# Kernel tuning notes

Measured on AMD Instinct MI355X. Metric: run time of the kernel, lower is better.

The kernel has to match this reference:

```python
import jax, jax.numpy as jnp
import numpy as np
import math

N, E, K_ORD = 30000, 60000, 6
D, H, DQK, PE_DIM, HYPER, MAX_K = 256, 8, 256, 128, 256, 10
DH = DQK // H    # per-head qk dim (dim_qk_head)
DVH = D // H     # per-head v dim  (dim_v_head)
M = E * K_ORD + N  # incidence messages + node self-loops


def _sin_pe(max_len, d):
    pos = np.arange(max_len)[:, None].astype(np.float32)
    div = np.exp(np.arange(0, d, 2).astype(np.float32) * (-math.log(10000.0) / d))
    pe = np.zeros((max_len, d), np.float32)
    pe[:, 0::2] = np.sin(pos * div)
    pe[:, 1::2] = np.cos(pos * div)
    return jnp.asarray(pe)


def _ln(x, g, b, eps=1e-5):
    mu = x.mean(-1, keepdims=True)
    var = ((x - mu) ** 2).mean(-1, keepdims=True)
    return (x - mu) * jax.lax.rsqrt(var + eps) * g + b


def _mlp(x, w1, b1, w2, b2):
    return jax.nn.relu(x @ w1 + b1) @ w2 + b2


def _forward(x_v, x_e, q_w1, q_b1, q_w2, q_b2, k_w, k_b, v_w, v_b,
             m1_w1, m1_b1, m1_w2, m1_b2, m2_w1, m2_b1, m2_w2, m2_b2,
             m3_w1, m3_b1, m3_w2, m3_b2, n1_g, n1_b, n2_g, n2_b, n3_g, n3_b,
             bias_v, edge_orders, edge_index):
    n = x_v.shape[0]
    # order-conditional positional MLP residual (pe1 at order 1 for nodes, edge_orders for edges)
    pe1 = _sin_pe(MAX_K + 1, D)
    x_v = x_v + _mlp(jnp.concatenate([_ln(x_v, n1_g, n1_b), jnp.broadcast_to(pe1[1], x_v.shape)], -1), m1_w1, m1_b1, m1_w2, m1_b2)
    x_e = x_e + _mlp(jnp.concatenate([_ln(x_e, n1_g, n1_b), pe1[edge_orders]], -1), m1_w1, m1_b1, m1_w2, m1_b2)

    # queries from PositionalMLP over positions {0, 1}
    q = _mlp(_sin_pe(2, PE_DIM), q_w1, q_b1, q_w2, q_b2)  # [2, DQK]
    q0 = q[0].reshape(H, DH)
    q1 = q[1].reshape(H, DH)

    tok = jnp.concatenate([x_e, x_v], 0)                    # [E+N, D], edges first
    k_all = tok @ k_w + k_b                                  # [E+N, 2*DQK]
    k0 = k_all[:, :DQK].reshape(-1, H, DH)
    k1 = k_all[:, DQK:].reshape(-1, H, DH)
    v = (tok @ v_w + v_b).reshape(-1, H, DVH)

    # global PMA: softmax over all edge+node tokens
    logit0 = jnp.einsum('hd,ehd->eh', q0, k0) / math.sqrt(DH)
    alpha0 = jax.nn.softmax(logit0, axis=0)
    att0 = jnp.einsum('eh,ehd->hd', alpha0, v).reshape(1, D)

    # segment PMA: leaky_relu -> scatter-softmax over messages per target node
    src, tgt = edge_index[0], edge_index[1]
    a = jnp.sum(k1 * q1[None], -1)                           # [E+N, H] (no sqrt scaling, per PMA)
    a = jax.nn.leaky_relu(a[src], 0.2)                       # [M, H]
    a_max = jax.ops.segment_max(a, tgt, num_segments=n)
    a = jnp.exp(a - a_max[tgt])
    a = a / jax.ops.segment_sum(a, tgt, num_segments=n)[tgt]
    att1 = jax.ops.segment_sum(v[src] * a[..., None], tgt, num_segments=n).reshape(n, D)

    pe2 = _sin_pe(2, D)
    att0 = att0 + _mlp(jnp.concatenate([_ln(att0, n2_g, n2_b), pe2[0:1]], -1), m2_w1, m2_b1, m2_w2, m2_b2)
    att1 = att1 + _mlp(jnp.concatenate([_ln(att1, n2_g, n2_b), jnp.broadcast_to(pe2[1], att1.shape)], -1), m2_w1, m2_b1, m2_w2, m2_b2)
    x = att0 + att1
    x = x + _mlp(_ln(x, n3_g, n3_b), m3_w1, m3_b1, m3_w2, m3_b2)
    return x + bias_v


def setup_inputs():
    key = jax.random.key(0)
    ks = jax.random.split(key, 64)
    idx = iter(range(64))
    def nrm(shape, fan_in=None):
        s = 1.0 if fan_in is None else 1.0 / math.sqrt(fan_in)
        return jax.random.normal(ks[next(idx)], shape, jnp.float32) * s
    inp = {}
    inp['x_v'] = nrm((N, D))
    inp['x_e'] = nrm((E, D))
    inp['edge_orders'] = jax.random.randint(ks[next(idx)], (E,), 2, MAX_K + 1)
    tgt_inc = jax.random.randint(ks[next(idx)], (E * K_ORD,), 0, N)
    src = jnp.concatenate([jnp.repeat(jnp.arange(E), K_ORD), E + jnp.arange(N)])
    tgt = jnp.concatenate([tgt_inc, jnp.arange(N)])
    inp['edge_index'] = jnp.stack([src, tgt]).astype(jnp.int32)
    inp['q_w1'] = nrm((PE_DIM, HYPER), PE_DIM); inp['q_b1'] = jnp.zeros((HYPER,), jnp.float32)
    inp['q_w2'] = nrm((HYPER, DQK), HYPER);     inp['q_b2'] = jnp.zeros((DQK,), jnp.float32)
    inp['k_w'] = nrm((D, 2 * DQK), D);          inp['k_b'] = jnp.zeros((2 * DQK,), jnp.float32)
    inp['v_w'] = nrm((D, D), D);                inp['v_b'] = jnp.zeros((D,), jnp.float32)
    inp['m1_w1'] = nrm((2 * D, HYPER), 2 * D);  inp['m1_b1'] = jnp.zeros((HYPER,), jnp.float32)
    inp['m1_w2'] = nrm((HYPER, D), HYPER);      inp['m1_b2'] = jnp.zeros((D,), jnp.float32)
    inp['m2_w1'] = nrm((2 * D, HYPER), 2 * D);  inp['m2_b1'] = jnp.zeros((HYPER,), jnp.float32)
    inp['m2_w2'] = nrm((HYPER, D), HYPER);      inp['m2_b2'] = jnp.zeros((D,), jnp.float32)
    inp['m3_w1'] = nrm((D, HYPER), D);          inp['m3_b1'] = jnp.zeros((HYPER,), jnp.float32)
    inp['m3_w2'] = nrm((HYPER, D), HYPER);      inp['m3_b2'] = jnp.zeros((D,), jnp.float32)
    for nm in ('n1', 'n2', 'n3'):
        inp[nm + '_g'] = jnp.ones((D,), jnp.float32)
        inp[nm + '_b'] = jnp.zeros((D,), jnp.float32)
    inp['bias_v'] = jnp.zeros((D,), jnp.float32)
    return inp


def reference(x_v, x_e, edge_orders, edge_index, q_w1, q_b1, q_w2, q_b2, k_w, k_b, v_w, v_b,
              m1_w1, m1_b1, m1_w2, m1_b2, m2_w1, m2_b1, m2_w2, m2_b2,
              m3_w1, m3_b1, m3_w2, m3_b2, n1_g, n1_b, n2_g, n2_b, n3_g, n3_b, bias_v):
    return _forward(x_v, x_e, q_w1, q_b1, q_w2, q_b2, k_w, k_b, v_w, v_b,
                    m1_w1, m1_b1, m1_w2, m1_b2, m2_w1, m2_b1, m2_w2, m2_b2,
                    m3_w1, m3_b1, m3_w2, m3_b2, n1_g, n1_b, n2_g, n2_b, n3_g, n3_b,
                    bias_v, edge_orders, edge_index)
```

## Files before the change

### kernel.cpp

```cpp
#include <hip/hip_runtime.h>
#include <hip/hip_bf16.h>

#define N_NODES 30000
#define N_EDGE  60000
#define T_TOK   90000
#define M_MSG   390000
#define DD      256
#define HH      8
#define AS      260
#define FUSED_BLKS 1407
#define HIST_BLKS  762
#define SCAT_BLKS 1524
#define RED_BLKS  176
#define ATT1_BLKS 7500

typedef unsigned short u16;
typedef unsigned int   u32;
typedef short s16x8 __attribute__((ext_vector_type(8)));
typedef float f32x4 __attribute__((ext_vector_type(4)));

constexpr size_t WS_V     = 0;
constexpr size_t WS_ALR   = WS_V    + (size_t)T_TOK * DD * 2;
constexpr size_t WS_CNT   = WS_ALR  + (size_t)T_TOK * HH * 4;
constexpr size_t WS_OFF   = WS_CNT  + (size_t)N_NODES * 4;
constexpr size_t WS_CUR   = WS_OFF  + (size_t)(N_NODES + 1) * 4;
constexpr size_t WS_MSRC  = WS_CUR  + (size_t)N_NODES * 4;
constexpr size_t WS_SMALL = ((WS_MSRC + (size_t)M_MSG * 4) + 255) & ~(size_t)255;

struct Small {
  u16 wts[16][256];
  float b0[8], b1f[8];
  float q[2][256];
  float pe_c1[11][256];
  float pc2[2][256];
  float gmaxv[8], ginv[8];
  float att0_vec[256];
  float att0_upd[256];
};
constexpr size_t WS_WTS  = (WS_SMALL + sizeof(Small) + 255) & ~(size_t)255;
constexpr size_t WS_PART = WS_WTS  + 7 * 65536 * 2;
constexpr size_t WS_PDEN = WS_PART + (size_t)FUSED_BLKS * 256 * 4;
constexpr size_t WS_PMAX = WS_PDEN + (size_t)FUSED_BLKS * 8 * 4;

__device__ __forceinline__ float bf2f(u16 a){ return __uint_as_float(((u32)a) << 16); }
__device__ __forceinline__ u32 pkbf(float lo, float hi){
  u32 r;
  asm("v_cvt_pk_bf16_f32 %0, %1, %2" : "=v"(r) : "v"(lo), "v"(hi));
  return r;
}
__device__ __forceinline__ u16 f2bf(float f){ return (u16)pkbf(f, f); }
__device__ __forceinline__ float wredsum(float x){
  #pragma unroll
  for (int s = 32; s > 0; s >>= 1) x += __shfl_xor(x, s, 64);
  return x;
}
__device__ __forceinline__ float wredmax(float x){
  #pragma unroll
  for (int s = 32; s > 0; s >>= 1) x = fmaxf(x, __shfl_xor(x, s, 64));
  return x;
}

union U8 { s16x8 v; uint2 u2[2]; uint4 u4; };

template<bool SC>
__device__ __forceinline__ void mfma_tile64(const u16* sa, const u16* __restrict__ WT,
                                            const u16* __restrict__ wts, int tid,
                                            f32x4 fr[4][2], f32x4* fs)
{
  const int lane = tid & 63, w = tid >> 6;
  const int l15 = lane & 15, g = lane >> 4;
  const int slab = w >> 1, nt0 = (w & 1) * 2;
  #pragma unroll
  for (int m = 0; m < 4; m++)
    #pragma unroll
    for (int n = 0; n < 2; n++) fr[m][n] = (f32x4){0.f, 0.f, 0.f, 0.f};
  const u16* ap = sa + l15 * AS + 4 * g;
  const u16* bp = WT + (size_t)slab * 16384 + lane * 8;
  const bool do_s = SC && (w == 0);
  #pragma unroll 4
  for (int c = 0; c < 8; c++){
    const int k0 = c * 32;
    U8 a[4];
    #pragma unroll
    for (int m = 0; m < 4; m++){
      a[m].u2[0] = *(const uint2*)(ap + m * 16 * AS + k0);
      a[m].u2[1] = *(const uint2*)(ap + m * 16 * AS + k0 + 16);
    }
    U8 b[2];
    #pragma unroll
    for (int n = 0; n < 2; n++)
      b[n].u4 = *(const uint4*)(bp + (c * 4 + nt0 + n) * 512);
    #pragma unroll
    for (int n = 0; n < 2; n++)
      #pragma unroll
      for (int m = 0; m < 4; m++)
        fr[m][n] = __builtin_amdgcn_mfma_f32_16x16x32_bf16(a[m].v, b[n].v, fr[m][n], 0, 0, 0);
    if (do_s){
      U8 bs;
      bs.u4 = *(const uint4*)(wts + c * 512 + lane * 8);
      #pragma unroll
      for (int m = 0; m < 4; m++)
        fs[m] = __builtin_amdgcn_mfma_f32_16x16x32_bf16(a[m].v, bs.v, fs[m], 0, 0, 0);
    }
  }
}

__global__ void k_preq(const float* __restrict__ qw1, const float* __restrict__ qb1,
                       const float* __restrict__ qw2, const float* __restrict__ qb2,
                       const float* __restrict__ kb, Small* sm, int* cnt)
{
  __shared__ float s_qin[2][128];
  __shared__ float s_h1[2][256];
  __shared__ float s_q[2][256];
  int tid = threadIdx.x;
  int p = tid >> 8, col = tid & 255;
  for (int i = tid; i < N_NODES; i += 512) cnt[i] = 0;
  if (tid < 256) sm->att0_vec[tid] = 0.f;
  if (tid < 128){
    int i = tid >> 1;
    float dv = expf((float)(2 * i) * (-9.210340371976184f / 128.f));
    if (tid & 1){ s_qin[0][tid] = 1.f; s_qin[1][tid] = cosf(dv); }
    else        { s_qin[0][tid] = 0.f; s_qin[1][tid] = sinf(dv); }
  }
  __syncthreads();
  {
    float acc = qb1[col];
    for (int d = 0; d < 128; d++) acc = fmaf(s_qin[p][d], qw1[d * 256 + col], acc);
    s_h1[p][col] = fmaxf(acc, 0.f);
  }
  __syncthreads();
  {
    float acc = qb2[col];
    for (int k = 0; k < 256; k++) acc = fmaf(s_h1[p][k], qw2[k * 256 + col], acc);
    s_q[p][col] = acc;
    sm->q[p][col] = acc;
  }
  __syncthreads();
  if (tid < 8){
    float b0 = 0.f, b1 = 0.f;
    for (int i = 0; i < 32; i++){
      b0 = fmaf(kb[tid * 32 + i],       s_q[0][tid * 32 + i], b0);
      b1 = fmaf(kb[256 + tid * 32 + i], s_q[1][tid * 32 + i], b1);
    }
    sm->b0[tid] = b0; sm->b1f[tid] = b1;
  }
}

__global__ void k_prep(const float* __restrict__ kw, const float* __restrict__ m1w1,
                       const float* __restrict__ m2w1, Small* sm,
                       const float* __restrict__ s0, const float* __restrict__ s1,
                       const float* __restrict__ s2, const float* __restrict__ s3,
                       const float* __restrict__ s4, const float* __restrict__ s5,
                       const float* __restrict__ s6, u16* __restrict__ dst)
{
  int role = blockIdx.x, tid = threadIdx.x;
  if (role < 8){
    int d = role * 32 + (tid >> 3), h = tid & 7;
    float a0 = 0.f, a1 = 0.f;
    #pragma unroll
    for (int i = 0; i < 32; i++){
      a0 = fmaf(kw[d * 512 + h * 32 + i],       sm->q[0][h * 32 + i], a0);
      a1 = fmaf(kw[d * 512 + 256 + h * 32 + i], sm->q[1][h * 32 + i], a1);
    }
    int c = d >> 5, kk = d & 31;
    int g = (kk & 15) >> 2;
    int j = (kk & 3) + ((kk & 16) ? 4 : 0);
    u16* wf = &sm->wts[0][0];
    wf[(c * 64 + g * 16 + h) * 8 + j]     = f2bf(a0);
    wf[(c * 64 + g * 16 + 8 + h) * 8 + j] = f2bf(a1);
  } else if (role < 19){
    __shared__ float s_pe[256];
    int o = role - 8;
    {
      int i = tid >> 1;
      float dv = expf((float)(2 * i) * (-9.210340371976184f / 256.f));
      float ph = (float)o * dv;
      s_pe[tid] = (tid & 1) ? cosf(ph) : sinf(ph);
    }
    __syncthreads();
    float acc = 0.f;
    for (int d = 0; d < 256; d++) acc = fmaf(s_pe[d], m1w1[(256 + d) * 256 + tid], acc);
    sm->pe_c1[o][tid] = acc;
  } else if (role == 19){
    __shared__ float p0[256], p1[256];
    {
      int i = tid >> 1;
      float dv = expf((float)(2 * i) * (-9.210340371976184f / 256.f));
      p0[tid] = (tid & 1) ? 1.f : 0.f;
      p1[tid] = (tid & 1) ? cosf(dv) : sinf(dv);
    }
    __syncthreads();
    float a0 = 0.f, a1 = 0.f;
    for (int d = 0; d < 256; d++){
      float w = m2w1[(256 + d) * 256 + tid];
      a0 = fmaf(p0[d], w, a0);
      a1 = fmaf(p1[d], w, a1);
    }
    sm->pc2[0][tid] = a0; sm->pc2[1][tid] = a1;
  } else {
    int b = role - 20;
    int mat = b >> 5, rem = b & 31;
    int slab = rem >> 3, c = rem & 7;
    const float* S;
    switch (mat){ case 0: S = s0; break; case 1: S = s1; break; case 2: S = s2; break;
                  case 3: S = s3; break; case 4: S = s4; break; case 5: S = s5; break;
                  default: S = s6; }
    int nt = tid >> 6, lane = tid & 63;
    int l15 = lane & 15, g = lane >> 4;
    int n = slab * 64 + nt * 16 + l15;
    u16 tmp[8];
    #pragma unroll
    for (int j = 0; j < 8; j++){
      int k = c * 32 + g * 4 + (j & 3) + ((j >= 4) ? 16 : 0);
      tmp[j] = f2bf(S[(size_t)k * 256 + n]);
    }
    uint4 o;
    o.x = (u32)tmp[0] | ((u32)tmp[1] << 16);
    o.y = (u32)tmp[2] | ((u32)tmp[3] << 16);
    o.z = (u32)tmp[4] | ((u32)tmp[5] << 16);
    o.w = (u32)tmp[6] | ((u32)tmp[7] << 16);
    *(uint4*)(dst + (size_t)mat * 65536 + (size_t)((((slab * 8 + c) * 4 + nt) * 64 + lane) * 8)) = o;
  }
}

__global__ __launch_bounds__(512, 4) void k_fused1(
    const float* __restrict__ x_v, const float* __restrict__ x_e,
    const int* __restrict__ edge_orders,
    const u16* __restrict__ WTa, const u16* __restrict__ WTb, const u16* __restrict__ WTv,
    const float* __restrict__ b1, const float* __restrict__ b2,
    const float* __restrict__ n1g, const float* __restrict__ n1b,
    const float* __restrict__ vb,
    const Small* __restrict__ sm,
    u16* __restrict__ v, float* __restrict__ alr,
    float* __restrict__ part, float* __restrict__ pden, float* __restrict__ pmax,
    const int* __restrict__ tgt, int* __restrict__ cnt)
{
  if (blockIdx.x >= FUSED_BLKS){
    int m = (blockIdx.x - FUSED_BLKS) * 512 + threadIdx.x;
    if (m < M_MSG) atomicAdd(&cnt[tgt[m]], 1);
    return;
  }
  __shared__ u16 s_a[64 * AS];
  __shared__ int s_ord[64];
  __shared__ float s_l[64][8];
  __shared__ float s_e[8][64];
  __shared__ float s_p2[512];
  const int tid = threadIdx.x;
  const int t0  = blockIdx.x * 64;
  const int w = tid >> 6, lane = tid & 63;
  const int l15 = lane & 15, g = lane >> 4;
  const int cb = w * 32;

  uint2 xp[8];
  {
    float4 gg = *(const float4*)(n1g + lane * 4);
    float4 bb = *(const float4*)(n1b + lane * 4);
    #pragma unroll
    for (int i = 0; i < 8; i++){
      int r = w * 8 + i;
      int t = t0 + r;
      float4 xv = make_float4(0.f, 0.f, 0.f, 0.f);
      if (t < T_TOK){
        const float* p = (t < N_EDGE) ? (x_e + (size_t)t * DD) : (x_v + (size_t)(t - N_EDGE) * DD);
        xv = *(const float4*)(p + lane * 4);
      }
      xp[i].x = pkbf(xv.x, xv.y);
      xp[i].y = pkbf(xv.z, xv.w);
      float s  = xv.x + xv.y + xv.z + xv.w;
      float ss = fmaf(xv.x, xv.x, fmaf(xv.y, xv.y, fmaf(xv.z, xv.z, xv.w * xv.w)));
      s = wredsum(s); ss = wredsum(ss);
      float mu  = s * (1.f / 256.f);
      float var = fmaf(-mu, mu, ss * (1.f / 256.f));
      float rs  = rsqrtf(var + 1e-5f);
      uint2 p2;
      p2.x = pkbf(fmaf((xv.x - mu) * rs, gg.x, bb.x), fmaf((xv.y - mu) * rs, gg.y, bb.y));
      p2.y = pkbf(fmaf((xv.z - mu) * rs, gg.z, bb.z), fmaf((xv.w - mu) * rs, gg.w, bb.w));
      *(uint2*)(s_a + r * AS + lane * 4) = p2;
    }
  }
  if (tid < 64){
    int t = t0 + tid;
    s_ord[tid] = (t < N_EDGE) ? edge_orders[t] : 1;
  }
  __syncthreads();

  f32x4 fr[4][2];
  mfma_tile64<false>(s_a, WTa, nullptr, tid, fr, nullptr);
  __syncthreads();
  {
    float b1c[2];
    #pragma unroll
    for (int n = 0; n < 2; n++) b1c[n] = b1[cb + n * 16 + l15];
    #pragma unroll
    for (int m = 0; m < 4; m++){
      #pragma unroll
      for (int r = 0; r < 4; r++){
        int row = m * 16 + 4 * g + r;
        const float* per = &sm->pe_c1[s_ord[row]][0];
        #pragma unroll
        for (int n = 0; n < 2; n++){
          int col = cb + n * 16 + l15;
          s_a[row * AS + col] = f2bf(fmaxf(fr[m][n][r] + b1c[n] + per[col], 0.f));
        }
      }
    }
  }
  __syncthreads();
  mfma_tile64<false>(s_a, WTb, nullptr, tid, fr, nullptr);
  __syncthreads();
  {
    float b2c[2];
    #pragma unroll
    for (int n = 0; n < 2; n++) b2c[n] = b2[cb + n * 16 + l15];
    #pragma unroll
    for (int m = 0; m < 4; m++)
      #pragma unroll
      for (int n = 0; n < 2; n++){
        int col = cb + n * 16 + l15;
        #pragma unroll
        for (int r = 0; r < 4; r++){
          int row = m * 16 + 4 * g + r;
          s_a[row * AS + col] = f2bf(fr[m][n][r] + b2c[n]);
        }
      }
  }
  __syncthreads();
  #pragma unroll
  for (int i = 0; i < 8; i++){
    int r = w * 8 + i;
    uint2 q = *(const uint2*)(s_a + r * AS + lane * 4);
    uint2 xq = xp[i];
    uint2 o;
    o.x = pkbf(bf2f((u16)(q.x & 0xffff)) + bf2f((u16)(xq.x & 0xffff)),
               bf2f((u16)(q.x >> 16))    + bf2f((u16)(xq.x >> 16)));
    o.y = pkbf(bf2f((u16)(q.y & 0xffff)) + bf2f((u16)(xq.y & 0xffff)),
               bf2f((u16)(q.y >> 16))    + bf2f((u16)(xq.y >> 16)));
    *(uint2*)(s_a + r * AS + lane * 4) = o;
  }
  __syncthreads();
  f32x4 fs[4];
  #pragma unroll
  for (int m = 0; m < 4; m++) fs[m] = (f32x4){0.f, 0.f, 0.f, 0.f};
  mfma_tile64<true>(s_a, WTv, &sm->wts[0][0], tid, fr, fs);
  __syncthreads();
  {
    float vbc[2];
    #pragma unroll
    for (int n = 0; n < 2; n++) vbc[n] = vb[cb + n * 16 + l15];
    #pragma unroll
    for (int m = 0; m < 4; m++)
      #pragma unroll
      for (int n = 0; n < 2; n++){
        int col = cb + n * 16 + l15;
        #pragma unroll
        for (int r = 0; r < 4; r++){
          int row = m * 16 + 4 * g + r;
          s_a[row * AS + col] = f2bf(fr[m][n][r] + vbc[n]);
        }
      }
  }
  if (w == 0){
    #pragma unroll
    for (int m = 0; m < 4; m++)
      #pragma unroll
      for (int r = 0; r < 4; r++){
        int row = m * 16 + 4 * g + r;
        int t = t0 + row;
        int sc = l15;
        if (sc < 8){
          float lv = (t < T_TOK) ? (fs[m][r] + sm->b0[sc]) * 0.17677669529663687f : -1e30f;
          s_l[row][sc] = lv;
        } else if (t < T_TOK){
          float a_ = fs[m][r] + sm->b1f[sc - 8];
          alr[(size_t)t * 8 + sc - 8] = (a_ > 0.f) ? a_ : 0.2f * a_;
        }
      }
  }
  __syncthreads();
  {
    float lv = s_l[lane][w];
    float mxb = wredmax(lv);
    float e = __expf(lv - mxb);
    float den = wredsum(e);
    s_e[w][lane] = e;
    if (lane == 0){
      pden[(size_t)blockIdx.x * 8 + w] = den;
      pmax[(size_t)blockIdx.x * 8 + w] = mxb;
    }
  }
  __syncthreads();
  {
    int col = tid & 255, half = tid >> 8;
    int h = col >> 5;
    float acc = 0.f;
    #pragma unroll 8
    for (int r2 = half * 32; r2 < half * 32 + 32; r2++)
      acc = fmaf(s_e[h][r2], bf2f(s_a[r2 * AS + col]), acc);
    s_p2[tid] = acc;
  }
  __syncthreads();
  if (tid < 256) part[(size_t)blockIdx.x * 256 + tid] = s_p2[tid] + s_p2[tid + 256];
  #pragma unroll
  for (int i = 0; i < 4; i++){
    int ch = i * 512 + tid;
    int r = ch >> 5, c8 = (ch & 31) * 8;
    int t = t0 + r;
    if (t < T_TOK){
      uint2 q0 = *(const uint2*)(s_a + r * AS + c8);
      uint2 q1 = *(const uint2*)(s_a + r * AS + c8 + 4);
      *(uint4*)(v + (size_t)t * DD + c8) = make_uint4(q0.x, q0.y, q1.x, q1.y);
    }
  }
}

__global__ __launch_bounds__(1024) void k_scanbc(
    const int* __restrict__ cnt, int* __restrict__ off, int* __restrict__ cur,
    const float* __restrict__ pden, const float* __restrict__ pmax,
    Small* sm)
{
  int tid = threadIdx.x;
  if (blockIdx.x == 0){
    __shared__ int s_s[1024];
    int base = tid * 30;
    int s = 0;
    if (tid < 1000){
      for (int i = 0; i < 30; i++) s += cnt[base + i];
    }
    s_s[tid] = s;
    __syncthreads();
    for (int ofs = 1; ofs < 1024; ofs <<= 1){
      int v_ = (tid >= ofs) ? s_s[tid - ofs] : 0;
      __syncthreads();
      s_s[tid] += v_;
      __syncthreads();
    }
    if (tid < 1000){
      int run = (tid == 0) ? 0 : s_s[tid - 1];
      for (int i = 0; i < 30; i++){
        int c = cnt[base + i];
        off[base + i] = run; cur[base + i] = run;
        run += c;
      }
    }
    if (tid == 0) off[N_NODES] = M_MSG;
    return;
  }
  __shared__ float s_red[1024];
  __shared__ float s_g[8];
  {
    int h = tid & 7, bi = tid >> 3;
    float m = -1e30f;
    for (int b = bi; b < FUSED_BLKS; b += 128) m = fmaxf(m, pmax[(size_t)b * 8 + h]);
    s_red[tid] = m;
  }
  __syncthreads();
  for (int s = 512; s >= 8; s >>= 1){ if (tid < s) s_red[tid] = fmaxf(s_red[tid], s_red[tid + s]); __syncthreads(); }
  if (tid < 8) s_g[tid] = s_red[tid];
  __syncthreads();
  {
    int h = tid & 7, bi = tid >> 3;
    float gm = s_g[h];
    float s = 0.f;
    for (int b = bi; b < FUSED_BLKS; b += 128)
      s += pden[(size_t)b * 8 + h] * __expf(pmax[(size_t)b * 8 + h] - gm);
    s_red[tid] = s;
  }
  __syncthreads();
  for (int s = 512; s >= 8; s >>= 1){ if (tid < s) s_red[tid] += s_red[tid + s]; __syncthreads(); }
  if (tid < 8){ sm->gmaxv[tid] = s_g[tid]; sm->ginv[tid] = 1.f / s_red[tid]; }
}

__global__ __launch_bounds__(256) void k_scatred(
    const int* __restrict__ src, const int* __restrict__ tgt,
    int* __restrict__ cur, int* __restrict__ msrc,
    const float* __restrict__ part, const float* __restrict__ pmax,
    Small* sm)
{
  int b = blockIdx.x, tid = threadIdx.x;
  if (b < SCAT_BLKS){
    int m = b * 256 + tid;
    if (m < M_MSG){
      int slot = atomicAdd(&cur[tgt[m]], 1);
      msrc[slot] = src[m];
    }
    return;
  }
  int r = b - SCAT_BLKS;
  int h = tid >> 5;
  float gm = sm->gmaxv[h];
  float acc = 0.f;
  #pragma unroll
  for (int j = 0; j < 8; j++){
    int pb = r * 8 + j;
    if (pb < FUSED_BLKS)
      acc = fmaf(part[(size_t)pb * 256 + tid], __expf(pmax[(size_t)pb * 8 + h] - gm), acc);
  }
  atomicAdd(&sm->att0_vec[tid], acc);
}

__global__ __launch_bounds__(256) void k_att1(
    const int* __restrict__ off, const int* __restrict__ msrc,
    const float* __restrict__ alr, const u16* __restrict__ v,
    const float* __restrict__ m2w1, const float* __restrict__ m2b1,
    const float* __restrict__ m2w2, const float* __restrict__ m2b2,
    const float* __restrict__ n2g, const float* __restrict__ n2b,
    Small* sm, float* att1)
{
  int tid = threadIdx.x;
  if (blockIdx.x == ATT1_BLKS){
    __shared__ float s_ln[256], s_h[256], s_r8[8];
    float x = sm->att0_vec[tid] * sm->ginv[tid >> 5];
    float s1 = wredsum(x), s2 = wredsum(x * x);
    int wv = tid >> 6;
    if ((tid & 63) == 0){ s_r8[wv] = s1; s_r8[4 + wv] = s2; }
    __syncthreads();
    float tot  = s_r8[0] + s_r8[1] + s_r8[2] + s_r8[3];
    float tot2 = s_r8[4] + s_r8[5] + s_r8[6] + s_r8[7];
    float mu  = tot * (1.f / 256.f);
    float var = tot2 * (1.f / 256.f) - mu * mu;
    float rs  = rsqrtf(var + 1e-5f);
    s_ln[tid] = (x - mu) * rs * n2g[tid] + n2b[tid];
    __syncthreads();
    float acc = m2b1[tid] + sm->pc2[0][tid];
    for (int k = 0; k < 256; k++) acc = fmaf(s_ln[k], m2w1[k * 256 + tid], acc);
    s_h[tid] = fmaxf(acc, 0.f);
    __syncthreads();
    float o = m2b2[tid];
    for (int k = 0; k < 256; k++) o = fmaf(s_h[k], m2w2[k * 256 + tid], o);
    sm->att0_upd[tid] = x + o;
    return;
  }
  int n = blockIdx.x * 4 + (tid >> 6);
  if (n >= N_NODES) return;
  int l = tid & 63;
  int h = l >> 3;
  int beg = off[n], end = off[n + 1];
  float mxa = -1e30f, mxb = -1e30f;
  int i = beg;
  for (; i + 1 < end; i += 2){
    mxa = fmaxf(mxa, alr[(size_t)msrc[i] * 8 + h]);
    mxb = fmaxf(mxb, alr[(size_t)msrc[i + 1] * 8 + h]);
  }
  if (i < end) mxa = fmaxf(mxa, alr[(size_t)msrc[i] * 8 + h]);
  float mx = fmaxf(mxa, mxb);
  float den0 = 0.f, den1 = 0.f;
  float a0 = 0.f, a1 = 0.f, a2 = 0.f, a3 = 0.f;
  float c0 = 0.f, c1 = 0.f, c2 = 0.f, c3 = 0.f;
  i = beg;
  for (; i + 1 < end; i += 2){
    int s0 = msrc[i], s1 = msrc[i + 1];
    float w0 = __expf(alr[(size_t)s0 * 8 + h] - mx);
    float w1 = __expf(alr[(size_t)s1 * 8 + h] - mx);
    ushort4 r0 = *(const ushort4*)(v + (size_t)s0 * DD + l * 4);
    ushort4 r1 = *(const ushort4*)(v + (size_t)s1 * DD + l * 4);
    den0 += w0; den1 += w1;
    a0 = fmaf(w0, bf2f(r0.x), a0); c0 = fmaf(w1, bf2f(r1.x), c0);
    a1 = fmaf(w0, bf2f(r0.y), a1); c1 = fmaf(w1, bf2f(r1.y), c1);
    a2 = fmaf(w0, bf2f(r0.z), a2); c2 = fmaf(w1, bf2f(r1.z), c2);
    a3 = fmaf(w0, bf2f(r0.w), a3); c3 = fmaf(w1, bf2f(r1.w), c3);
  }
  if (i < end){
    int s0 = msrc[i];
    float w0 = __expf(alr[(size_t)s0 * 8 + h] - mx);
    ushort4 r0 = *(const ushort4*)(v + (size_t)s0 * DD + l * 4);
    den0 += w0;
    a0 = fmaf(w0, bf2f(r0.x), a0);
    a1 = fmaf(w0, bf2f(r0.y), a1);
    a2 = fmaf(w0, bf2f(r0.z), a2);
    a3 = fmaf(w0, bf2f(r0.w), a3);
  }
  float id_ = 1.f / (den0 + den1);
  *(float4*)(att1 + (size_t)n * DD + l * 4) =
      make_float4((a0 + c0) * id_, (a1 + c1) * id_, (a2 + c2) * id_, (a3 + c3) * id_);
}

__global__ __launch_bounds__(512, 4) void k_final(
    const float* att1,
    const u16* __restrict__ WT2a, const u16* __restrict__ WT2b,
    const u16* __restrict__ WT3a, const u16* __restrict__ WT3b,
    const float* __restrict__ m2b1, const float* __restrict__ m2b2,
    const float* __restrict__ m3b1, const float* __restrict__ m3b2,
    const float* __restrict__ n2g, const float* __restrict__ n2b,
    const float* __restrict__ n3g, const float* __restrict__ n3b,
    const float* __restrict__ bias_v, const Small* __restrict__ sm,
    float* out)
{
  __shared__ u16 s_a[64 * AS];
  const int tid = threadIdx.x;
  const int t0  = blockIdx.x * 64;
  const int w = tid >> 6, lane = tid & 63;
  const int l15 = lane & 15, g = lane >> 4;
  const int cb = w * 32;

  f32x4 xr[8];
  {
    float4 gg = *(const float4*)(n2g + lane * 4);
    float4 bb = *(const float4*)(n2b + lane * 4);
    #pragma unroll
    for (int i = 0; i < 8; i++){
      int r = w * 8 + i;
      int t = t0 + r;
      float4 xv = make_float4(0.f, 0.f, 0.f, 0.f);
      if (t < N_NODES) xv = *(const float4*)(att1 + (size_t)t * DD + lane * 4);
      xr[i][0] = xv.x; xr[i][1] = xv.y; xr[i][2] = xv.z; xr[i][3] = xv.w;
      float s  = xv.x + xv.y + xv.z + xv.w;
      float ss = fmaf(xv.x, xv.x, fmaf(xv.y, xv.y, fmaf(xv.z, xv.z, xv.w * xv.w)));
      s = wredsum(s); ss = wredsum(ss);
      float mu  = s * (1.f / 256.f);
      float var = fmaf(-mu, mu, ss * (1.f / 256.f));
      float rs  = rsqrtf(var + 1e-5f);
      uint2 p2;
      p2.x = pkbf(fmaf((xv.x - mu) * rs, gg.x, bb.x), fmaf((xv.y - mu) * rs, gg.y, bb.y));
      p2.y = pkbf(fmaf((xv.z - mu) * rs, gg.z, bb.z), fmaf((xv.w - mu) * rs, gg.w, bb.w));
      *(uint2*)(s_a + r * AS + lane * 4) = p2;
    }
  }
  __syncthreads();

  f32x4 fr[4][2];
  mfma_tile64<false>(s_a, WT2a, nullptr, tid, fr, nullptr);
  __syncthreads();
  {
    float bc[2], pc[2];
    #pragma unroll
    for (int n = 0; n < 2; n++){
      int col = cb + n * 16 + l15;
      bc[n] = m2b1[col]; pc[n] = sm->pc2[1][col];
    }
    #pragma unroll
    for (int m = 0; m < 4; m++)
      #pragma unroll
      for (int n = 0; n < 2; n++){
        int col = cb + n * 16 + l15;
        #pragma unroll
        for (int r = 0; r < 4; r++){
          int row = m * 16 + 4 * g + r;
          s_a[row * AS + col] = f2bf(fmaxf(fr[m][n][r] + bc[n] + pc[n], 0.f));
        }
      }
  }
  __syncthreads();
  mfma_tile64<false>(s_a, WT2b, nullptr, tid, fr, nullptr);
  __syncthreads();
  {
    float bc[2], ac[2];
    #pragma unroll
    for (int n = 0; n < 2; n++){
      int col = cb + n * 16 + l15;
      bc[n] = m2b2[col]; ac[n] = sm->att0_upd[col];
    }
    #pragma unroll
    for (int m = 0; m < 4; m++)
      #pragma unroll
      for (int n = 0; n < 2; n++){
        int col = cb + n * 16 + l15;
        #pragma unroll
        for (int r = 0; r < 4; r++){
          int row = m * 16 + 4 * g + r;
          s_a[row * AS + col] = f2bf(fr[m][n][r] + bc[n] + ac[n]);
        }
      }
  }
  __syncthreads();
  {
    float4 gg = *(const float4*)(n3g + lane * 4);
    float4 bb = *(const float4*)(n3b + lane * 4);
    #pragma unroll
    for (int i = 0; i < 8; i++){
      int r = w * 8 + i;
      uint2 q = *(const uint2*)(s_a + r * AS + lane * 4);
      float x0 = xr[i][0] + bf2f((u16)(q.x & 0xffff));
      float x1 = xr[i][1] + bf2f((u16)(q.x >> 16));
      float x2 = xr[i][2] + bf2f((u16)(q.y & 0xffff));
      float x3 = xr[i][3] + bf2f((u16)(q.y >> 16));
      xr[i][0] = x0; xr[i][1] = x1; xr[i][2] = x2; xr[i][3] = x3;
      float s  = x0 + x1 + x2 + x3;
      float ss = fmaf(x0, x0, fmaf(x1, x1, fmaf(x2, x2, x3 * x3)));
      s = wredsum(s); ss = wredsum(ss);
      float mu  = s * (1.f / 256.f);
      float var = fmaf(-mu, mu, ss * (1.f / 256.f));
      float rs  = rsqrtf(var + 1e-5f);
      uint2 p2;
      p2.x = pkbf(fmaf((x0 - mu) * rs, gg.x, bb.x), fmaf((x1 - mu) * rs, gg.y, bb.y));
      p2.y = pkbf(fmaf((x2 - mu) * rs, gg.z, bb.z), fmaf((x3 - mu) * rs, gg.w, bb.w));
      *(uint2*)(s_a + r * AS + lane * 4) = p2;
    }
  }
  __syncthreads();
  mfma_tile64<false>(s_a, WT3a, nullptr, tid, fr, nullptr);
  __syncthreads();
  {
    float bc[2];
    #pragma unroll
    for (int n = 0; n < 2; n++) bc[n] = m3b1[cb + n * 16 + l15];
    #pragma unroll
    for (int m = 0; m < 4; m++)
      #pragma unroll
      for (int n = 0; n < 2; n++){
        int col = cb + n * 16 + l15;
        #pragma unroll
        for (int r = 0; r < 4; r++){
          int row = m * 16 + 4 * g + r;
          s_a[row * AS + col] = f2bf(fmaxf(fr[m][n][r] + bc[n], 0.f));
        }
      }
  }
  __syncthreads();
  mfma_tile64<false>(s_a, WT3b, nullptr, tid, fr, nullptr);
  __syncthreads();
  {
    float bc[2];
    #pragma unroll
    for (int n = 0; n < 2; n++){
      int col = cb + n * 16 + l15;
      bc[n] = m3b2[col] + bias_v[col];
    }
    #pragma unroll
    for (int m = 0; m < 4; m++)
      #pragma unroll
      for (int n = 0; n < 2; n++){
        int col = cb + n * 16 + l15;
        #pragma unroll
        for (int r = 0; r < 4; r++){
          int row = m * 16 + 4 * g + r;
          s_a[row * AS + col] = f2bf(fr[m][n][r] + bc[n]);
        }
      }
  }
  __syncthreads();
  #pragma unroll
  for (int i = 0; i < 8; i++){
    int r = w * 8 + i;
    int t = t0 + r;
    if (t < N_NODES){
      uint2 q = *(const uint2*)(s_a + r * AS + lane * 4);
      float4 o;
      o.x = xr[i][0] + bf2f((u16)(q.x & 0xffff));
      o.y = xr[i][1] + bf2f((u16)(q.x >> 16));
      o.z = xr[i][2] + bf2f((u16)(q.y & 0xffff));
      o.w = xr[i][3] + bf2f((u16)(q.y >> 16));
      *(float4*)(out + (size_t)t * DD + lane * 4) = o;
    }
  }
}

extern "C" void kernel_launch(void* const* d_in, const int* in_sizes, int n_in,
                              void* d_out, int out_size, void* d_ws, size_t ws_size,
                              hipStream_t stream)
{
  const float* x_v = (const float*)d_in[0];
  const float* x_e = (const float*)d_in[1];
  const int* edge_orders = (const int*)d_in[2];
  const int* edge_index  = (const int*)d_in[3];
  const float* q_w1 = (const float*)d_in[4],  *q_b1 = (const float*)d_in[5];
  const float* q_w2 = (const float*)d_in[6],  *q_b2 = (const float*)d_in[7];
  const float* k_w  = (const float*)d_in[8],  *k_b  = (const float*)d_in[9];
  const float* v_w  = (const float*)d_in[10], *v_b  = (const float*)d_in[11];
  const float* m1w1 = (const float*)d_in[12], *m1b1 = (const float*)d_in[13];
  const float* m1w2 = (const float*)d_in[14], *m1b2 = (const float*)d_in[15];
  const float* m2w1 = (const float*)d_in[16], *m2b1 = (const float*)d_in[17];
  const float* m2w2 = (const float*)d_in[18], *m2b2 = (const float*)d_in[19];
  const float* m3w1 = (const float*)d_in[20], *m3b1 = (const float*)d_in[21];
  const float* m3w2 = (const float*)d_in[22], *m3b2 = (const float*)d_in[23];
  const float* n1g = (const float*)d_in[24], *n1b = (const float*)d_in[25];
  const float* n2g = (const float*)d_in[26], *n2b = (const float*)d_in[27];
  const float* n3g = (const float*)d_in[28], *n3b = (const float*)d_in[29];
  const float* bias_v = (const float*)d_in[30];

  char* ws = (char*)d_ws;
  u16*   v      = (u16*)  (ws + WS_V);
  float* alr    = (float*)(ws + WS_ALR);
  int*   cnt    = (int*)  (ws + WS_CNT);
  int*   off    = (int*)  (ws + WS_OFF);
  int*   cur    = (int*)  (ws + WS_CUR);
  int*   msrc   = (int*)  (ws + WS_MSRC);
  Small* sm     = (Small*)(ws + WS_SMALL);
  u16*   wtb    = (u16*)  (ws + WS_WTS);
  float* part   = (float*)(ws + WS_PART);
  float* pden   = (float*)(ws + WS_PDEN);
  float* pmax   = (float*)(ws + WS_PMAX);
  const int* src = edge_index;
  const int* tgt = edge_index + M_MSG;
  float* att1 = (float*)d_out;
  float* out  = (float*)d_out;

  k_preq<<<1, 512, 0, stream>>>(q_w1, q_b1, q_w2, q_b2, k_b, sm, cnt);
  k_prep<<<244, 256, 0, stream>>>(k_w, m1w1, m2w1, sm,
                                  m1w1, m1w2, v_w, m2w1, m2w2, m3w1, m3w2, wtb);
  k_fused1<<<FUSED_BLKS + HIST_BLKS, 512, 0, stream>>>(x_v, x_e, edge_orders,
                                                  wtb + 0 * 65536, wtb + 1 * 65536, wtb + 2 * 65536,
                                                  m1b1, m1b2, n1g, n1b, v_b, sm, v, alr,
                                                  part, pden, pmax, tgt, cnt);
  k_scanbc<<<2, 1024, 0, stream>>>(cnt, off, cur, pden, pmax, sm);
  k_scatred<<<SCAT_BLKS + RED_BLKS, 256, 0, stream>>>(src, tgt, cur, msrc, part, pmax, sm);
  k_att1<<<ATT1_BLKS + 1, 256, 0, stream>>>(off, msrc, alr, v,
                                            m2w1, m2b1, m2w2, m2b2, n2g, n2b, sm, att1);
  k_final<<<(N_NODES + 63) / 64, 512, 0, stream>>>(att1,
                                                   wtb + 3 * 65536, wtb + 4 * 65536,
                                                   wtb + 5 * 65536, wtb + 6 * 65536,
                                                   m2b1, m2b2, m3b1, m3b2,
                                                   n2g, n2b, n3g, n3b, bias_v, sm, out);
}
```

Measured before the change: 245.6 us.

## Fuse segment-softmax aggregation into final MLP kernel and fold att0 update into scatter

The per-node segment softmax aggregation that used to run as its own kernel (k_att1) now runs inside k_final's load phase, so att1 never goes to global memory and is never reloaded. The global att0 LayerNorm/MLP update moves into k_scatred's reduction blocks and is run by the last block to finish, found with a done counter and threadfence. This drops one launch and a 30000x256 fp32 round trip. In exchange, k_final blocks (64 nodes, 512 threads) now do irregular gathers serially per wave over 8 nodes, which may cut latency hiding compared with the finer 4-nodes-per-block grid used before.

```diff
diff --git a/kernel.cpp b/kernel.cpp
--- a/kernel.cpp
+++ b/kernel.cpp
@@ -12,7 +12,6 @@
 #define HIST_BLKS  762
 #define SCAT_BLKS 1524
 #define RED_BLKS  176
-#define ATT1_BLKS 7500
 
 typedef unsigned short u16;
 typedef unsigned int   u32;
@@ -36,6 +35,7 @@
   float gmaxv[8], ginv[8];
   float att0_vec[256];
   float att0_upd[256];
+  int   done;
 };
 constexpr size_t WS_WTS  = (WS_SMALL + sizeof(Small) + 255) & ~(size_t)255;
 constexpr size_t WS_PART = WS_WTS  + 7 * 65536 * 2;
@@ -116,6 +116,7 @@
   int p = tid >> 8, col = tid & 255;
   for (int i = tid; i < N_NODES; i += 512) cnt[i] = 0;
   if (tid < 256) sm->att0_vec[tid] = 0.f;
+  if (tid == 0) sm->done = 0;
   if (tid < 128){
     int i = tid >> 1;
     float dv = expf((float)(2 * i) * (-9.210340371976184f / 128.f));
@@ -474,6 +475,9 @@
     const int* __restrict__ src, const int* __restrict__ tgt,
     int* __restrict__ cur, int* __restrict__ msrc,
     const float* __restrict__ part, const float* __restrict__ pmax,
+    const float* __restrict__ m2w1, const float* __restrict__ m2b1,
+    const float* __restrict__ m2w2, const float* __restrict__ m2b2,
+    const float* __restrict__ n2g, const float* __restrict__ n2b,
     Small* sm)
 {
   int b = blockIdx.x, tid = threadIdx.x;
@@ -496,86 +500,37 @@
       acc = fmaf(part[(size_t)pb * 256 + tid], __expf(pmax[(size_t)pb * 8 + h] - gm), acc);
   }
   atomicAdd(&sm->att0_vec[tid], acc);
-}
-
-__global__ __launch_bounds__(256) void k_att1(
+  __shared__ int s_last;
+  __threadfence();
+  __syncthreads();
+  if (tid == 0) s_last = (atomicAdd(&sm->done, 1) == RED_BLKS - 1) ? 1 : 0;
+  __syncthreads();
+  if (!s_last) return;
+  __shared__ float s_ln[256], s_h[256], s_r8[8];
+  float x = atomicAdd(&sm->att0_vec[tid], 0.f) * sm->ginv[tid >> 5];
+  float s1 = wredsum(x), s2 = wredsum(x * x);
+  int wv = tid >> 6;
+  if ((tid & 63) == 0){ s_r8[wv] = s1; s_r8[4 + wv] = s2; }
+  __syncthreads();
+  float tot  = s_r8[0] + s_r8[1] + s_r8[2] + s_r8[3];
+  float tot2 = s_r8[4] + s_r8[5] + s_r8[6] + s_r8[7];
+  float mu  = tot * (1.f / 256.f);
+  float var = tot2 * (1.f / 256.f) - mu * mu;
+  float rs  = rsqrtf(var + 1e-5f);
+  s_ln[tid] = (x - mu) * rs * n2g[tid] + n2b[tid];
+  __syncthreads();
+  float acc1 = m2b1[tid] + sm->pc2[0][tid];
+  for (int k = 0; k < 256; k++) acc1 = fmaf(s_ln[k], m2w1[k * 256 + tid], acc1);
+  s_h[tid] = fmaxf(acc1, 0.f);
+  __syncthreads();
+  float o = m2b2[tid];
+  for (int k = 0; k < 256; k++) o = fmaf(s_h[k], m2w2[k * 256 + tid], o);
+  sm->att0_upd[tid] = x + o;
+}
+
+__global__ __launch_bounds__(512, 4) void k_final(
     const int* __restrict__ off, const int* __restrict__ msrc,
     const float* __restrict__ alr, const u16* __restrict__ v,
-    const float* __restrict__ m2w1, const float* __restrict__ m2b1,
-    const float* __restrict__ m2w2, const float* __restrict__ m2b2,
-    const float* __restrict__ n2g, const float* __restrict__ n2b,
-    Small* sm, float* att1)
-{
-  int tid = threadIdx.x;
-  if (blockIdx.x == ATT1_BLKS){
-    __shared__ float s_ln[256], s_h[256], s_r8[8];
-    float x = sm->att0_vec[tid] * sm->ginv[tid >> 5];
-    float s1 = wredsum(x), s2 = wredsum(x * x);
-    int wv = tid >> 6;
-    if ((tid & 63) == 0){ s_r8[wv] = s1; s_r8[4 + wv] = s2; }
-    __syncthreads();
-    float tot  = s_r8[0] + s_r8[1] + s_r8[2] + s_r8[3];
-    float tot2 = s_r8[4] + s_r8[5] + s_r8[6] + s_r8[7];
-    float mu  = tot * (1.f / 256.f);
-    float var = tot2 * (1.f / 256.f) - mu * mu;
-    float rs  = rsqrtf(var + 1e-5f);
-    s_ln[tid] = (x - mu) * rs * n2g[tid] + n2b[tid];
-    __syncthreads();
-    float acc = m2b1[tid] + sm->pc2[0][tid];
-    for (int k = 0; k < 256; k++) acc = fmaf(s_ln[k], m2w1[k * 256 + tid], acc);
-    s_h[tid] = fmaxf(acc, 0.f);
-    __syncthreads();
-    float o = m2b2[tid];
-    for (int k = 0; k < 256; k++) o = fmaf(s_h[k], m2w2[k * 256 + tid], o);
-    sm->att0_upd[tid] = x + o;
-    return;
-  }
-  int n = blockIdx.x * 4 + (tid >> 6);
-  if (n >= N_NODES) return;
-  int l = tid & 63;
-  int h = l >> 3;
-  int beg = off[n], end = off[n + 1];
-  float mxa = -1e30f, mxb = -1e30f;
-  int i = beg;
-  for (; i + 1 < end; i += 2){
-    mxa = fmaxf(mxa, alr[(size_t)msrc[i] * 8 + h]);
-    mxb = fmaxf(mxb, alr[(size_t)msrc[i + 1] * 8 + h]);
-  }
-  if (i < end) mxa = fmaxf(mxa, alr[(size_t)msrc[i] * 8 + h]);
-  float mx = fmaxf(mxa, mxb);
-  float den0 = 0.f, den1 = 0.f;
-  float a0 = 0.f, a1 = 0.f, a2 = 0.f, a3 = 0.f;
-  float c0 = 0.f, c1 = 0.f, c2 = 0.f, c3 = 0.f;
-  i = beg;
-  for (; i + 1 < end; i += 2){
-    int s0 = msrc[i], s1 = msrc[i + 1];
-    float w0 = __expf(alr[(size_t)s0 * 8 + h] - mx);
-    float w1 = __expf(alr[(size_t)s1 * 8 + h] - mx);
-    ushort4 r0 = *(const ushort4*)(v + (size_t)s0 * DD + l * 4);
-    ushort4 r1 = *(const ushort4*)(v + (size_t)s1 * DD + l * 4);
-    den0 += w0; den1 += w1;
-    a0 = fmaf(w0, bf2f(r0.x), a0); c0 = fmaf(w1, bf2f(r1.x), c0);
-    a1 = fmaf(w0, bf2f(r0.y), a1); c1 = fmaf(w1, bf2f(r1.y), c1);
-    a2 = fmaf(w0, bf2f(r0.z), a2); c2 = fmaf(w1, bf2f(r1.z), c2);
-    a3 = fmaf(w0, bf2f(r0.w), a3); c3 = fmaf(w1, bf2f(r1.w), c3);
-  }
-  if (i < end){
-    int s0 = msrc[i];
-    float w0 = __expf(alr[(size_t)s0 * 8 + h] - mx);
-    ushort4 r0 = *(const ushort4*)(v + (size_t)s0 * DD + l * 4);
-    den0 += w0;
-    a0 = fmaf(w0, bf2f(r0.x), a0);
-    a1 = fmaf(w0, bf2f(r0.y), a1);
-    a2 = fmaf(w0, bf2f(r0.z), a2);
-    a3 = fmaf(w0, bf2f(r0.w), a3);
-  }
-  float id_ = 1.f / (den0 + den1);
-  *(float4*)(att1 + (size_t)n * DD + l * 4) =
-      make_float4((a0 + c0) * id_, (a1 + c1) * id_, (a2 + c2) * id_, (a3 + c3) * id_);
-}
-
-__global__ __launch_bounds__(512, 4) void k_final(
-    const float* att1,
     const u16* __restrict__ WT2a, const u16* __restrict__ WT2b,
     const u16* __restrict__ WT3a, const u16* __restrict__ WT3b,
     const float* __restrict__ m2b1, const float* __restrict__ m2b2,
@@ -591,6 +546,7 @@
   const int w = tid >> 6, lane = tid & 63;
   const int l15 = lane & 15, g = lane >> 4;
   const int cb = w * 32;
+  const int h = lane >> 3;
 
   f32x4 xr[8];
   {
@@ -598,20 +554,59 @@
     float4 bb = *(const float4*)(n2b + lane * 4);
     #pragma unroll
     for (int i = 0; i < 8; i++){
-      int r = w * 8 + i;
-      int t = t0 + r;
-      float4 xv = make_float4(0.f, 0.f, 0.f, 0.f);
-      if (t < N_NODES) xv = *(const float4*)(att1 + (size_t)t * DD + lane * 4);
-      xr[i][0] = xv.x; xr[i][1] = xv.y; xr[i][2] = xv.z; xr[i][3] = xv.w;
-      float s  = xv.x + xv.y + xv.z + xv.w;
-      float ss = fmaf(xv.x, xv.x, fmaf(xv.y, xv.y, fmaf(xv.z, xv.z, xv.w * xv.w)));
+      int n = t0 + w * 8 + i;
+      float r0o = 0.f, r1o = 0.f, r2o = 0.f, r3o = 0.f;
+      if (n < N_NODES){
+        int beg = off[n], end = off[n + 1];
+        float mxa = -1e30f, mxb = -1e30f;
+        int j = beg;
+        for (; j + 1 < end; j += 2){
+          mxa = fmaxf(mxa, alr[(size_t)msrc[j] * 8 + h]);
+          mxb = fmaxf(mxb, alr[(size_t)msrc[j + 1] * 8 + h]);
+        }
+        if (j < end) mxa = fmaxf(mxa, alr[(size_t)msrc[j] * 8 + h]);
+        float mx = fmaxf(mxa, mxb);
+        float den0 = 0.f, den1 = 0.f;
+        float a0 = 0.f, a1 = 0.f, a2 = 0.f, a3 = 0.f;
+        float c0 = 0.f, c1 = 0.f, c2 = 0.f, c3 = 0.f;
+        j = beg;
+        for (; j + 1 < end; j += 2){
+          int s0 = msrc[j], s1 = msrc[j + 1];
+          float w0 = __expf(alr[(size_t)s0 * 8 + h] - mx);
+          float w1 = __expf(alr[(size_t)s1 * 8 + h] - mx);
+          ushort4 q0 = *(const ushort4*)(v + (size_t)s0 * DD + lane * 4);
+          ushort4 q1 = *(const ushort4*)(v + (size_t)s1 * DD + lane * 4);
+          den0 += w0; den1 += w1;
+          a0 = fmaf(w0, bf2f(q0.x), a0); c0 = fmaf(w1, bf2f(q1.x), c0);
+          a1 = fmaf(w0, bf2f(q0.y), a1); c1 = fmaf(w1, bf2f(q1.y), c1);
+          a2 = fmaf(w0, bf2f(q0.z), a2); c2 = fmaf(w1, bf2f(q1.z), c2);
+          a3 = fmaf(w0, bf2f(q0.w), a3); c3 = fmaf(w1, bf2f(q1.w), c3);
+        }
+        if (j < end){
+          int s0 = msrc[j];
+          float w0 = __expf(alr[(size_t)s0 * 8 + h] - mx);
+          ushort4 q0 = *(const ushort4*)(v + (size_t)s0 * DD + lane * 4);
+          den0 += w0;
+          a0 = fmaf(w0, bf2f(q0.x), a0);
+          a1 = fmaf(w0, bf2f(q0.y), a1);
+          a2 = fmaf(w0, bf2f(q0.z), a2);
+          a3 = fmaf(w0, bf2f(q0.w), a3);
+        }
+        float id_ = 1.f / (den0 + den1);
+        r0o = (a0 + c0) * id_; r1o = (a1 + c1) * id_;
+        r2o = (a2 + c2) * id_; r3o = (a3 + c3) * id_;
+      }
+      xr[i][0] = r0o; xr[i][1] = r1o; xr[i][2] = r2o; xr[i][3] = r3o;
+      float s  = r0o + r1o + r2o + r3o;
+      float ss = fmaf(r0o, r0o, fmaf(r1o, r1o, fmaf(r2o, r2o, r3o * r3o)));
       s = wredsum(s); ss = wredsum(ss);
       float mu  = s * (1.f / 256.f);
       float var = fmaf(-mu, mu, ss * (1.f / 256.f));
       float rs  = rsqrtf(var + 1e-5f);
+      int r = w * 8 + i;
       uint2 p2;
-      p2.x = pkbf(fmaf((xv.x - mu) * rs, gg.x, bb.x), fmaf((xv.y - mu) * rs, gg.y, bb.y));
-      p2.y = pkbf(fmaf((xv.z - mu) * rs, gg.z, bb.z), fmaf((xv.w - mu) * rs, gg.w, bb.w));
+      p2.x = pkbf(fmaf((r0o - mu) * rs, gg.x, bb.x), fmaf((r1o - mu) * rs, gg.y, bb.y));
+      p2.y = pkbf(fmaf((r2o - mu) * rs, gg.z, bb.z), fmaf((r3o - mu) * rs, gg.w, bb.w));
       *(uint2*)(s_a + r * AS + lane * 4) = p2;
     }
   }
@@ -781,7 +776,6 @@
   float* pmax   = (float*)(ws + WS_PMAX);
   const int* src = edge_index;
   const int* tgt = edge_index + M_MSG;
-  float* att1 = (float*)d_out;
   float* out  = (float*)d_out;
 
   k_preq<<<1, 512, 0, stream>>>(q_w1, q_b1, q_w2, q_b2, k_b, sm, cnt);
@@ -792,10 +786,9 @@
                                                   m1b1, m1b2, n1g, n1b, v_b, sm, v, alr,
                                                   part, pden, pmax, tgt, cnt);
   k_scanbc<<<2, 1024, 0, stream>>>(cnt, off, cur, pden, pmax, sm);
-  k_scatred<<<SCAT_BLKS + RED_BLKS, 256, 0, stream>>>(src, tgt, cur, msrc, part, pmax, sm);
-  k_att1<<<ATT1_BLKS + 1, 256, 0, stream>>>(off, msrc, alr, v,
-                                            m2w1, m2b1, m2w2, m2b2, n2g, n2b, sm, att1);
-  k_final<<<(N_NODES + 63) / 64, 512, 0, stream>>>(att1,
+  k_scatred<<<SCAT_BLKS + RED_BLKS, 256, 0, stream>>>(src, tgt, cur, msrc, part, pmax,
+                                                      m2w1, m2b1, m2w2, m2b2, n2g, n2b, sm);
+  k_final<<<(N_NODES + 63) / 64, 512, 0, stream>>>(off, msrc, alr, v,
                                                    wtb + 3 * 65536, wtb + 4 * 65536,
                                                    wtb + 5 * 65536, wtb + 6 * 65536,
                                                    m2b1, m2b2, m3b1, m3b2,
```

New measurement: 292.6 us. +19.1%, slower.
